# Kernel optimization log

Measured on AMD Instinct MI355X. Metric: run time of the kernel, lower is better.

The kernel has to match this reference:

```python
import jax, jax.numpy as jnp
import numpy as np
import math

H = 128
W = 128
N = 2048
DIM = 768
TWO_PI = 2.0 * math.pi
ALPHA_MIN = 1.0 / 255.0


def setup_inputs() -> dict:
    key = jax.random.key(0)
    ks = jax.random.split(key, 6)
    # _xyz = atanh(2*(rand-0.5)); clip uniform away from endpoints to avoid inf
    u = jax.random.uniform(ks[0], (N, 2), minval=1e-4, maxval=1.0 - 1e-4)
    xyz = jnp.arctanh(2.0 * (u - 0.5))
    scaling = jax.random.uniform(ks[1], (N, 2))
    rotation = jax.random.uniform(ks[2], (N, 1))
    features = jax.random.uniform(ks[3], (N, 3))
    opacity = jnp.ones((N, 1), jnp.float32)
    w_up = jax.random.normal(ks[4], (DIM, 3), jnp.float32) * 0.05
    b_up = jnp.zeros((DIM,), jnp.float32)
    x = jax.random.normal(ks[5], (1, DIM, H, W), jnp.float32)
    return {"x": x, "xyz": xyz, "scaling": scaling, "rotation": rotation,
            "features": features, "opacity": opacity, "w_up": w_up, "b_up": b_up}


def _forward(xyz, scaling, rotation, features, opacity, w_up, b_up):
    # activations (get_xyz / get_scaling / get_rotation)
    means = jnp.tanh(xyz)                                   # [N,2] in (-1,1)
    s = jnp.abs(scaling + 0.5)                              # [N,2]
    theta = jax.nn.sigmoid(rotation[:, 0]) * TWO_PI         # [N]
    c, sn = jnp.cos(theta), jnp.sin(theta)
    # M = R(theta) @ diag(s); cov2d = M M^T
    a = c * s[:, 0]; b = -sn * s[:, 1]
    d = sn * s[:, 0]; e = c * s[:, 1]
    cov_xx = a * a + b * b
    cov_xy = a * d + b * e
    cov_yy = d * d + e * e
    det = cov_xx * cov_yy - cov_xy * cov_xy
    # conic = inverse covariance (A, B, C)
    A = cov_yy / det; B = -cov_xy / det; C = cov_xx / det   # [N]
    # project [-1,1] -> pixel centers
    gx = 0.5 * (means[:, 0] + 1.0) * W                      # [N]
    gy = 0.5 * (means[:, 1] + 1.0) * H
    px = jnp.arange(W, dtype=jnp.float32) + 0.5
    py = jnp.arange(H, dtype=jnp.float32) + 0.5
    PX, PY = jnp.meshgrid(px, py)                           # [H,W], PX varies along W
    dx = gx[None, :] - PX.reshape(-1)[:, None]              # [P,N], P=H*W
    dy = gy[None, :] - PY.reshape(-1)[:, None]
    sigma = 0.5 * (A * dx * dx + C * dy * dy) + B * dx * dy # [P,N]
    alpha = jnp.minimum(0.999, opacity[:, 0][None, :] * jnp.exp(-sigma))
    alpha = jnp.where((sigma < 0.0) | (alpha < ALPHA_MIN), 0.0, alpha)
    # summation rasterizer: per-pixel weighted sum of colors
    img = jnp.clip(alpha @ features, 0.0, 1.0)              # [P,3]
    feat = img @ w_up.T + b_up                              # [P,DIM]
    return feat.T.reshape(1, DIM, H, W)


def reference(x, xyz, scaling, rotation, features, opacity, w_up, b_up):
    del x  # only its channel dim (== DIM) shapes the output in the original
    return _forward(xyz, scaling, rotation, features, opacity, w_up, b_up)
```

## Files before the change

### kernel.cpp

```cpp
#include <hip/hip_runtime.h>
#include <math.h>

#define HH 128
#define WW 128
#define NG 2048
#define DIMV 768
#define PIX (HH * WW)
#define A_MIN (1.0f / 255.0f)
#define TW 16
#define TH 4
#define TWO_PI 6.28318530717958647692f

__global__ __launch_bounds__(256) void raster_kernel(
    const float* __restrict__ xyz, const float* __restrict__ scaling,
    const float* __restrict__ rotation, const float* __restrict__ features,
    const float* __restrict__ opacity, float* __restrict__ img)
{
    __shared__ float4 sP0[NG];
    __shared__ float4 sP1[NG];
    __shared__ float2 sP2[NG];
    __shared__ int s_cnt;
    __shared__ int s_list[NG];
    __shared__ float s_red[4 * 64 * 3];

    int tid = threadIdx.x;
    int bx = blockIdx.x & 7, by = blockIdx.x >> 3;
    int px0 = bx * TW, py0 = by * TH;

    if (tid == 0) s_cnt = 0;

    for (int g = tid; g < NG; g += 256) {
        float2 xz = ((const float2*)xyz)[g];
        float e2x = __expf(2.0f * xz.x);
        float e2y = 2.0f * __expf(2.0f * xz.y);
        float gx = (e2x / (e2x + 1.0f)) * (float)WW;
        float gy = (e2y / (e2y + 2.0f)) * (float)HH;
        float2 sc = ((const float2*)scaling)[g];
        float s0 = fabsf(sc.x + 0.5f);
        float s1 = fabsf(sc.y + 0.5f);
        float th = TWO_PI / (1.0f + __expf(-rotation[g]));
        float sn = __sinf(th), cs = __cosf(th);
        float a = cs * s0, b = -sn * s1, d = sn * s0, e = cs * s1;
        float cxx = a * a + b * b;
        float cxy = a * d + b * e;
        float cyy = d * d + e * e;
        float inv = 1.0f / (cxx * cyy - cxy * cxy);
        float op = opacity[g];
        float L = __logf(255.0f * op);
        float r2 = (L > 0.0f) ? 2.0f * L * (cxx + cyy) * 1.0002f + 1e-3f : -1.0f;
        sP0[g] = make_float4(0.5f * cyy * inv, -cxy * inv, 0.5f * cxx * inv, op);
        sP1[g] = make_float4(gx, gy, features[3 * g + 0], features[3 * g + 1]);
        sP2[g] = make_float2(features[3 * g + 2], r2);
    }
    __syncthreads();

    {
        float x0 = px0 + 0.5f, x1 = px0 + TW - 0.5f;
        float y0 = py0 + 0.5f, y1 = py0 + TH - 0.5f;
        for (int g = tid; g < NG; g += 256) {
            float4 c1 = sP1[g];
            float2 c2 = sP2[g];
            float ddx = fmaxf(fmaxf(x0 - c1.x, c1.x - x1), 0.0f);
            float ddy = fmaxf(fmaxf(y0 - c1.y, c1.y - y1), 0.0f);
            if (ddx * ddx + ddy * ddy <= c2.y) {
                int pos = atomicAdd(&s_cnt, 1);
                s_list[pos] = g;
            }
        }
    }
    __syncthreads();
    int cnt = s_cnt;

    int lane = tid & 63, wv = tid >> 6;
    float pxf = px0 + (lane & 15) + 0.5f;
    float pyf = py0 + (lane >> 4) + 0.5f;

    float ar = 0.0f, ag = 0.0f, ab = 0.0f;
    for (int k = wv; k < cnt; k += 4) {
        int g = __builtin_amdgcn_readfirstlane(s_list[k]);
        float4 a0 = sP0[g];
        float4 a1 = sP1[g];
        float2 a2 = sP2[g];
        float dx = a1.x - pxf, dy = a1.y - pyf;
        float sig = fmaf(a0.y * dx, dy, fmaf(a0.x * dx, dx, a0.z * dy * dy));
        float al = fminf(0.999f, a0.w * __expf(-sig));
        al = (sig < 0.0f || al < A_MIN) ? 0.0f : al;
        ar = fmaf(al, a1.z, ar);
        ag = fmaf(al, a1.w, ag);
        ab = fmaf(al, a2.x, ab);
    }
    s_red[(wv * 64 + lane) * 3 + 0] = ar;
    s_red[(wv * 64 + lane) * 3 + 1] = ag;
    s_red[(wv * 64 + lane) * 3 + 2] = ab;
    __syncthreads();

    if (tid < 64) {
        float sr = 0.0f, sg = 0.0f, sb = 0.0f;
        #pragma unroll
        for (int w = 0; w < 4; ++w) {
            sr += s_red[(w * 64 + tid) * 3 + 0];
            sg += s_red[(w * 64 + tid) * 3 + 1];
            sb += s_red[(w * 64 + tid) * 3 + 2];
        }
        int p = (py0 + (tid >> 4)) * WW + px0 + (tid & 15);
        img[p]           = fminf(1.0f, fmaxf(0.0f, sr));
        img[PIX + p]     = fminf(1.0f, fmaxf(0.0f, sg));
        img[2 * PIX + p] = fminf(1.0f, fmaxf(0.0f, sb));
    }
}

__global__ __launch_bounds__(256) void project_kernel(
    const float* __restrict__ img, const float* __restrict__ w_up,
    const float* __restrict__ b_up, float* __restrict__ out)
{
    int grp = blockIdx.x >> 4;
    int seg = blockIdx.x & 15;
    int p = seg * 1024 + threadIdx.x * 4;
    float4 r = *(const float4*)(img + p);
    float4 g = *(const float4*)(img + PIX + p);
    float4 b = *(const float4*)(img + 2 * PIX + p);
    int d0 = grp * 4;
    #pragma unroll
    for (int i = 0; i < 4; ++i) {
        int d = d0 + i;
        float w0 = w_up[3 * d + 0], w1 = w_up[3 * d + 1], w2 = w_up[3 * d + 2];
        float bb = b_up[d];
        float4 v;
        v.x = fmaf(w0, r.x, fmaf(w1, g.x, fmaf(w2, b.x, bb)));
        v.y = fmaf(w0, r.y, fmaf(w1, g.y, fmaf(w2, b.y, bb)));
        v.z = fmaf(w0, r.z, fmaf(w1, g.z, fmaf(w2, b.z, bb)));
        v.w = fmaf(w0, r.w, fmaf(w1, g.w, fmaf(w2, b.w, bb)));
        *(float4*)(out + (size_t)d * PIX + p) = v;
    }
}

extern "C" void kernel_launch(void* const* d_in, const int* in_sizes, int n_in,
                              void* d_out, int out_size, void* d_ws, size_t ws_size,
                              hipStream_t stream)
{
    const float* xyz      = (const float*)d_in[1];
    const float* scaling  = (const float*)d_in[2];
    const float* rotation = (const float*)d_in[3];
    const float* features = (const float*)d_in[4];
    const float* opacity  = (const float*)d_in[5];
    const float* w_up     = (const float*)d_in[6];
    const float* b_up     = (const float*)d_in[7];
    float* out = (float*)d_out;
    float* img = (float*)d_ws;

    raster_kernel<<<256, 256, 0, stream>>>(xyz, scaling, rotation, features,
                                           opacity, img);
    project_kernel<<<(DIMV / 4) * 16, 256, 0, stream>>>(img, w_up, b_up, out);
}
```

Measured before the change: 113.7 us.

## Fuse rasterizer and projection into one kernel with per-tile culled parameter chunks

```diff
diff --git a/kernel.cpp b/kernel.cpp
--- a/kernel.cpp
+++ b/kernel.cpp
@@ -9,62 +9,56 @@
 #define A_MIN (1.0f / 255.0f)
 #define TW 16
 #define TH 4
+#define NT 512
+#define NWV 8
+#define CH 256
 #define TWO_PI 6.28318530717958647692f
 
-__global__ __launch_bounds__(256) void raster_kernel(
+__global__ __launch_bounds__(NT) void fused_kernel(
     const float* __restrict__ xyz, const float* __restrict__ scaling,
     const float* __restrict__ rotation, const float* __restrict__ features,
-    const float* __restrict__ opacity, float* __restrict__ img)
+    const float* __restrict__ opacity, const float* __restrict__ w_up,
+    const float* __restrict__ b_up, float* __restrict__ out)
 {
-    __shared__ float4 sP0[NG];
-    __shared__ float4 sP1[NG];
-    __shared__ float2 sP2[NG];
     __shared__ int s_cnt;
-    __shared__ int s_list[NG];
-    __shared__ float s_red[4 * 64 * 3];
+    __shared__ int s_idx[NG];
+    __shared__ float4 cA[CH];
+    __shared__ float4 cB[CH];
+    __shared__ float2 cC[CH];
+    __shared__ float s_red[NWV * 64 * 3];
+    __shared__ __align__(16) float s_r[64];
+    __shared__ __align__(16) float s_g[64];
+    __shared__ __align__(16) float s_b[64];
 
     int tid = threadIdx.x;
     int bx = blockIdx.x & 7, by = blockIdx.x >> 3;
     int px0 = bx * TW, py0 = by * TH;
 
     if (tid == 0) s_cnt = 0;
-
-    for (int g = tid; g < NG; g += 256) {
-        float2 xz = ((const float2*)xyz)[g];
-        float e2x = __expf(2.0f * xz.x);
-        float e2y = 2.0f * __expf(2.0f * xz.y);
-        float gx = (e2x / (e2x + 1.0f)) * (float)WW;
-        float gy = (e2y / (e2y + 2.0f)) * (float)HH;
-        float2 sc = ((const float2*)scaling)[g];
-        float s0 = fabsf(sc.x + 0.5f);
-        float s1 = fabsf(sc.y + 0.5f);
-        float th = TWO_PI / (1.0f + __expf(-rotation[g]));
-        float sn = __sinf(th), cs = __cosf(th);
-        float a = cs * s0, b = -sn * s1, d = sn * s0, e = cs * s1;
-        float cxx = a * a + b * b;
-        float cxy = a * d + b * e;
-        float cyy = d * d + e * e;
-        float inv = 1.0f / (cxx * cyy - cxy * cxy);
-        float op = opacity[g];
-        float L = __logf(255.0f * op);
-        float r2 = (L > 0.0f) ? 2.0f * L * (cxx + cyy) * 1.0002f + 1e-3f : -1.0f;
-        sP0[g] = make_float4(0.5f * cyy * inv, -cxy * inv, 0.5f * cxx * inv, op);
-        sP1[g] = make_float4(gx, gy, features[3 * g + 0], features[3 * g + 1]);
-        sP2[g] = make_float2(features[3 * g + 2], r2);
-    }
     __syncthreads();
 
     {
         float x0 = px0 + 0.5f, x1 = px0 + TW - 0.5f;
         float y0 = py0 + 0.5f, y1 = py0 + TH - 0.5f;
-        for (int g = tid; g < NG; g += 256) {
-            float4 c1 = sP1[g];
-            float2 c2 = sP2[g];
-            float ddx = fmaxf(fmaxf(x0 - c1.x, c1.x - x1), 0.0f);
-            float ddy = fmaxf(fmaxf(y0 - c1.y, c1.y - y1), 0.0f);
-            if (ddx * ddx + ddy * ddy <= c2.y) {
+        #pragma unroll
+        for (int g0 = 0; g0 < NG; g0 += NT) {
+            int g = g0 + tid;
+            float2 xz = ((const float2*)xyz)[g];
+            float e2x = __expf(2.0f * xz.x);
+            float e2y = 2.0f * __expf(2.0f * xz.y);
+            float gx = (e2x / (e2x + 1.0f)) * (float)WW;
+            float gy = (e2y / (e2y + 2.0f)) * (float)HH;
+            float2 sc = ((const float2*)scaling)[g];
+            float s0 = fabsf(sc.x + 0.5f);
+            float s1 = fabsf(sc.y + 0.5f);
+            float trc = s0 * s0 + s1 * s1;
+            float L = __logf(255.0f * opacity[g]);
+            float r2 = (L > 0.0f) ? 2.0f * L * trc * 1.0002f + 1e-3f : -1.0f;
+            float ddx = fmaxf(fmaxf(x0 - gx, gx - x1), 0.0f);
+            float ddy = fmaxf(fmaxf(y0 - gy, gy - y1), 0.0f);
+            if (ddx * ddx + ddy * ddy <= r2) {
                 int pos = atomicAdd(&s_cnt, 1);
-                s_list[pos] = g;
+                s_idx[pos] = g;
             }
         }
     }
@@ -74,63 +68,82 @@
     int lane = tid & 63, wv = tid >> 6;
     float pxf = px0 + (lane & 15) + 0.5f;
     float pyf = py0 + (lane >> 4) + 0.5f;
+    float ar = 0.0f, ag = 0.0f, ab = 0.0f;
 
-    float ar = 0.0f, ag = 0.0f, ab = 0.0f;
-    for (int k = wv; k < cnt; k += 4) {
-        int g = __builtin_amdgcn_readfirstlane(s_list[k]);
-        float4 a0 = sP0[g];
-        float4 a1 = sP1[g];
-        float2 a2 = sP2[g];
-        float dx = a1.x - pxf, dy = a1.y - pyf;
-        float sig = fmaf(a0.y * dx, dy, fmaf(a0.x * dx, dx, a0.z * dy * dy));
-        float al = fminf(0.999f, a0.w * __expf(-sig));
-        al = (sig < 0.0f || al < A_MIN) ? 0.0f : al;
-        ar = fmaf(al, a1.z, ar);
-        ag = fmaf(al, a1.w, ag);
-        ab = fmaf(al, a2.x, ab);
+    for (int ck = 0; ck < cnt; ck += CH) {
+        int csz = min(CH, cnt - ck);
+        for (int j = tid; j < csz; j += NT) {
+            int g = s_idx[ck + j];
+            float2 xz = ((const float2*)xyz)[g];
+            float e2x = __expf(2.0f * xz.x);
+            float e2y = 2.0f * __expf(2.0f * xz.y);
+            float gx = (e2x / (e2x + 1.0f)) * (float)WW;
+            float gy = (e2y / (e2y + 2.0f)) * (float)HH;
+            float2 sc = ((const float2*)scaling)[g];
+            float s0 = fabsf(sc.x + 0.5f);
+            float s1 = fabsf(sc.y + 0.5f);
+            float th = TWO_PI / (1.0f + __expf(-rotation[g]));
+            float sn = __sinf(th), cs = __cosf(th);
+            float a = cs * s0, b = -sn * s1, d = sn * s0, e = cs * s1;
+            float cxx = a * a + b * b;
+            float cxy = a * d + b * e;
+            float cyy = d * d + e * e;
+            float inv = 1.0f / (cxx * cyy - cxy * cxy);
+            float op = opacity[g];
+            cA[j] = make_float4(0.5f * cyy * inv, -cxy * inv, 0.5f * cxx * inv, op);
+            cB[j] = make_float4(gx, gy, features[3 * g + 0], features[3 * g + 1]);
+            cC[j] = make_float2(features[3 * g + 2], 0.0f);
+        }
+        __syncthreads();
+        for (int k = wv; k < csz; k += NWV) {
+            float4 a0 = cA[k];
+            float4 a1 = cB[k];
+            float2 a2 = cC[k];
+            float dx = a1.x - pxf, dy = a1.y - pyf;
+            float sig = fmaf(a0.y * dx, dy, fmaf(a0.x * dx, dx, a0.z * dy * dy));
+            float al = fminf(0.999f, a0.w * __expf(-sig));
+            al = (sig < 0.0f || al < A_MIN) ? 0.0f : al;
+            ar = fmaf(al, a1.z, ar);
+            ag = fmaf(al, a1.w, ag);
+            ab = fmaf(al, a2.x, ab);
+        }
+        __syncthreads();
     }
+
     s_red[(wv * 64 + lane) * 3 + 0] = ar;
     s_red[(wv * 64 + lane) * 3 + 1] = ag;
     s_red[(wv * 64 + lane) * 3 + 2] = ab;
     __syncthreads();
-
     if (tid < 64) {
         float sr = 0.0f, sg = 0.0f, sb = 0.0f;
         #pragma unroll
-        for (int w = 0; w < 4; ++w) {
+        for (int w = 0; w < NWV; ++w) {
             sr += s_red[(w * 64 + tid) * 3 + 0];
             sg += s_red[(w * 64 + tid) * 3 + 1];
             sb += s_red[(w * 64 + tid) * 3 + 2];
         }
-        int p = (py0 + (tid >> 4)) * WW + px0 + (tid & 15);
-        img[p]           = fminf(1.0f, fmaxf(0.0f, sr));
-        img[PIX + p]     = fminf(1.0f, fmaxf(0.0f, sg));
-        img[2 * PIX + p] = fminf(1.0f, fmaxf(0.0f, sb));
+        s_r[tid] = fminf(1.0f, fmaxf(0.0f, sr));
+        s_g[tid] = fminf(1.0f, fmaxf(0.0f, sg));
+        s_b[tid] = fminf(1.0f, fmaxf(0.0f, sb));
     }
-}
+    __syncthreads();
 
-__global__ __launch_bounds__(256) void project_kernel(
-    const float* __restrict__ img, const float* __restrict__ w_up,
-    const float* __restrict__ b_up, float* __restrict__ out)
-{
-    int grp = blockIdx.x >> 4;
-    int seg = blockIdx.x & 15;
-    int p = seg * 1024 + threadIdx.x * 4;
-    float4 r = *(const float4*)(img + p);
-    float4 g = *(const float4*)(img + PIX + p);
-    float4 b = *(const float4*)(img + 2 * PIX + p);
-    int d0 = grp * 4;
-    #pragma unroll
-    for (int i = 0; i < 4; ++i) {
-        int d = d0 + i;
+    int q = tid & 15, dbase = tid >> 4;
+    int row = q >> 2, c4 = q & 3;
+    float4 r4 = *(const float4*)&s_r[row * 16 + c4 * 4];
+    float4 g4 = *(const float4*)&s_g[row * 16 + c4 * 4];
+    float4 b4 = *(const float4*)&s_b[row * 16 + c4 * 4];
+    size_t pofs = (size_t)(py0 + row) * WW + px0 + c4 * 4;
+    for (int i = 0; i < DIMV / 32; ++i) {
+        int d = dbase + (i << 5);
         float w0 = w_up[3 * d + 0], w1 = w_up[3 * d + 1], w2 = w_up[3 * d + 2];
         float bb = b_up[d];
         float4 v;
-        v.x = fmaf(w0, r.x, fmaf(w1, g.x, fmaf(w2, b.x, bb)));
-        v.y = fmaf(w0, r.y, fmaf(w1, g.y, fmaf(w2, b.y, bb)));
-        v.z = fmaf(w0, r.z, fmaf(w1, g.z, fmaf(w2, b.z, bb)));
-        v.w = fmaf(w0, r.w, fmaf(w1, g.w, fmaf(w2, b.w, bb)));
-        *(float4*)(out + (size_t)d * PIX + p) = v;
+        v.x = fmaf(w0, r4.x, fmaf(w1, g4.x, fmaf(w2, b4.x, bb)));
+        v.y = fmaf(w0, r4.y, fmaf(w1, g4.y, fmaf(w2, b4.y, bb)));
+        v.z = fmaf(w0, r4.z, fmaf(w1, g4.z, fmaf(w2, b4.z, bb)));
+        v.w = fmaf(w0, r4.w, fmaf(w1, g4.w, fmaf(w2, b4.w, bb)));
+        *(float4*)(out + (size_t)d * PIX + pofs) = v;
     }
 }
 
@@ -145,10 +158,8 @@
     const float* opacity  = (const float*)d_in[5];
     const float* w_up     = (const float*)d_in[6];
     const float* b_up     = (const float*)d_in[7];
-    float* out = (float*)d_out;
-    float* img = (float*)d_ws;
+    (void)d_ws; (void)ws_size;
 
-    raster_kernel<<<256, 256, 0, stream>>>(xyz, scaling, rotation, features,
-                                           opacity, img);
-    project_kernel<<<(DIMV / 4) * 16, 256, 0, stream>>>(img, w_up, b_up, out);
+    fused_kernel<<<256, NT, 0, stream>>>(xyz, scaling, rotation, features,
+                                         opacity, w_up, b_up, (float*)d_out);
 }
```

After: 126.6 us. +11.4%, slower.
